# Performance work log

Measured on AMD Instinct MI355X. Metric: run time of the kernel, lower is better.

The kernel has to match this reference:

```python
import jax, jax.numpy as jnp
import numpy as np

B, T, D, H = 4, 2048, 1024, 16


def setup_inputs() -> dict:
    key = jax.random.key(0)
    ks = jax.random.split(key, 5)
    s = 0.02  # keep activations sane
    return {
        "x": jax.random.normal(ks[0], (B, T, D), jnp.float32),
        "Wq": jax.random.normal(ks[1], (D, D), jnp.float32) * s,
        "bq": jnp.zeros((D,), jnp.float32),
        "Wk": jax.random.normal(ks[2], (D, D), jnp.float32) * s,
        "bk": jnp.zeros((D,), jnp.float32),
        "Wv": jax.random.normal(ks[3], (D, D), jnp.float32) * s,
        "bv": jnp.zeros((D,), jnp.float32),
        "Wo": jax.random.normal(ks[4], (D, D), jnp.float32) * s,
        "bo": jnp.zeros((D,), jnp.float32),
    }


def _split_heads(t):  # (B,T,D) -> (B,H,T,d)
    b, s, d = t.shape
    return t.reshape(b, s, H, d // H).transpose(0, 2, 1, 3)


def reference(x, Wq, bq, Wk, bk, Wv, bv, Wo, bo):
    d_k = D // H
    q = _split_heads(x @ Wq + bq)  # (B,H,T,d)
    k = _split_heads(x @ Wk + bk)
    v = _split_heads(x @ Wv + bv)
    # scaled dot-product similarities (B,H,T,T)
    scores = jnp.einsum("bhqd,bhkd->bhqk", q, k) / jnp.sqrt(jnp.asarray(d_k, x.dtype))
    # causal mask: masked_fill(tril==0, -inf)
    causal = jnp.tril(jnp.ones((T, T), bool))
    scores = jnp.where(causal, scores, -jnp.inf)
    attn = jax.nn.softmax(scores, axis=-1)
    ctx = jnp.einsum("bhqk,bhkd->bhqd", attn, v)  # (B,H,T,d)
    ctx = ctx.transpose(0, 2, 1, 3).reshape(x.shape[0], T, D)
    return ctx @ Wo + bo
```

## Files before the change

kernel.cpp:

```cpp
#include <hip/hip_runtime.h>
#include <hip/hip_bf16.h>

typedef unsigned short u16;
typedef __attribute__((ext_vector_type(8))) short bf16x8;
typedef __attribute__((ext_vector_type(4))) short bf16x4;
typedef __attribute__((ext_vector_type(4))) float f32x4;

#define DD 1024
#define TT 2048
#define HH 16
#define BB 4
#define DK 64
#define MM 8192

#define QSCALE 0.180336880f

__device__ __forceinline__ u16 f2b(float x) {
  __hip_bfloat16 h = __float2bfloat16(x);
  return *reinterpret_cast<u16*>(&h);
}

__device__ __forceinline__ unsigned pk2(float a, float b) {
  float2 t; t.x = a; t.y = b;
  __hip_bfloat162 h = __float22bfloat162_rn(t);
  union { __hip_bfloat162 h; unsigned u; } cv;
  cv.h = h;
  return cv.u;
}

#define GLD16(gp, lp)                                                         \
  __builtin_amdgcn_global_load_lds(                                           \
      (const __attribute__((address_space(1))) unsigned int*)(gp),            \
      (__attribute__((address_space(3))) unsigned int*)(lp), 16, 0, 0)

__global__ __launch_bounds__(256) void cast_bf16_kernel(
    const float* __restrict__ src, u16* __restrict__ dst, int n) {
  int i = (blockIdx.x * 256 + threadIdx.x) * 4;
  if (i + 3 < n) {
    float4 v = *reinterpret_cast<const float4*>(src + i);
    ushort4 o;
    o.x = f2b(v.x); o.y = f2b(v.y); o.z = f2b(v.z); o.w = f2b(v.w);
    *reinterpret_cast<ushort4*>(dst + i) = o;
  }
}

__global__ __launch_bounds__(256) void transpose_cast_kernel(
    const float* __restrict__ W0, const float* __restrict__ W1,
    const float* __restrict__ W2, const float* __restrict__ W3,
    u16* __restrict__ O0, u16* __restrict__ O1,
    u16* __restrict__ O2, u16* __restrict__ O3) {
  const float* W; u16* O;
  switch (blockIdx.z) {
    case 0: W = W0; O = O0; break;
    case 1: W = W1; O = O1; break;
    case 2: W = W2; O = O2; break;
    default: W = W3; O = O3; break;
  }
  __shared__ float tile[32][33];
  int tx = threadIdx.x, ty = threadIdx.y;
  int bx = blockIdx.x * 32;
  int by = blockIdx.y * 32;
#pragma unroll
  for (int j = 0; j < 4; j++)
    tile[ty + j * 8][tx] = W[(size_t)(by + ty + j * 8) * DD + bx + tx];
  __syncthreads();
#pragma unroll
  for (int j = 0; j < 4; j++)
    O[(size_t)(bx + ty + j * 8) * DD + by + tx] = f2b(tile[tx][ty + j * 8]);
}

#define GEMM_STAGE(Aptr, Bptr, Asl, Bsl)                                      \
  _Pragma("unroll") for (int c = 0; c < 4; c++) {                             \
    int idx = tid * 8 + c * 2048;                                             \
    int row = idx >> 6, ck = idx & 63;                                        \
    int src = ck ^ ((row & 7) << 3);                                          \
    GLD16(Aptr + (size_t)(m0 + row) * DD + k0 + src, Asl + idx);              \
    GLD16(Bptr + (size_t)(n0 + row) * DD + k0 + src, Bsl + idx);              \
  }

#define GEMM_MFMA(Asl, Bsl)                                                   \
  _Pragma("unroll") for (int half = 0; half < 2; half++) {                    \
    bf16x8 af[4], bfr[4];                                                     \
    _Pragma("unroll") for (int mb = 0; mb < 4; mb++) {                        \
      int r = wm + mb * 16 + l16;                                             \
      af[mb] = *reinterpret_cast<const bf16x8*>(                              \
          &Asl[r * 64 + ((half * 32 + quad * 8) ^ ((r & 7) << 3))]);          \
    }                                                                         \
    _Pragma("unroll") for (int nb = 0; nb < 4; nb++) {                        \
      int r = wn + nb * 16 + l16;                                             \
      bfr[nb] = *reinterpret_cast<const bf16x8*>(                             \
          &Bsl[r * 64 + ((half * 32 + quad * 8) ^ ((r & 7) << 3))]);          \
    }                                                                         \
    _Pragma("unroll") for (int mb = 0; mb < 4; mb++)                          \
      _Pragma("unroll") for (int nb = 0; nb < 4; nb++)                        \
          acc[mb][nb] = __builtin_amdgcn_mfma_f32_16x16x32_bf16(              \
              af[mb], bfr[nb], acc[mb][nb], 0, 0, 0);                         \
  }

__global__ __launch_bounds__(256, 4) void gemm_qkv_kernel(
    const u16* __restrict__ A,
    const u16* __restrict__ WtQ, const u16* __restrict__ WtK,
    const u16* __restrict__ WtV,
    const float* __restrict__ bq, const float* __restrict__ bk,
    const float* __restrict__ bv,
    u16* __restrict__ Qo, u16* __restrict__ Ko, u16* __restrict__ Vo) {
  __shared__ __align__(16) u16 smem[17408];
  u16* As = smem;
  u16* Bs = smem + 8192;
  u16* Vs = smem;
  int z = blockIdx.z;
  const u16* Bt = (z == 0) ? WtQ : ((z == 1) ? WtK : WtV);
  const float* bias = (z == 0) ? bq : ((z == 1) ? bk : bv);
  int tid = threadIdx.x;
  int wave = tid >> 6, lane = tid & 63;
  int quad = lane >> 4, l16 = lane & 15;
  int m0 = blockIdx.x * 128, n0 = blockIdx.y * 128;
  int wm = (wave >> 1) * 64, wn = (wave & 1) * 64;

  f32x4 acc[4][4];
#pragma unroll
  for (int i = 0; i < 4; i++)
#pragma unroll
    for (int j = 0; j < 4; j++) acc[i][j] = (f32x4){0.f, 0.f, 0.f, 0.f};

  for (int k0 = 0; k0 < DD; k0 += 64) {
    GEMM_STAGE(A, Bt, As, Bs)
    __syncthreads();
    GEMM_MFMA(As, Bs)
    __syncthreads();
  }

  if (z == 2) {
#pragma unroll
    for (int mb = 0; mb < 4; mb++)
#pragma unroll
      for (int nb = 0; nb < 4; nb++) {
        int col = wn + nb * 16 + l16;
        float bv2 = bias[n0 + col];
#pragma unroll
        for (int r = 0; r < 4; r++) {
          int row = wm + mb * 16 + quad * 4 + r;
          Vs[col * 136 + row] = f2b(acc[mb][nb][r] + bv2);
        }
      }
    __syncthreads();
    int b = m0 >> 11;
    int tloc = m0 & 2047;
#pragma unroll
    for (int i = 0; i < 8; i++) {
      int idx = tid * 8 + i * 2048;
      int row = idx >> 7, col = idx & 127;
      uint4 v = *reinterpret_cast<const uint4*>(&Vs[row * 136 + col]);
      int ncol = n0 + row, h = ncol >> 6, dd = ncol & 63;
      *reinterpret_cast<uint4*>(
          Vo + (((size_t)(b * HH + h) * DK) + dd) * TT + tloc + col) = v;
    }
    return;
  }

  u16* outp = (z == 0) ? Qo : Ko;
  float scale = (z == 0) ? QSCALE : 1.0f;
#pragma unroll
  for (int mb = 0; mb < 4; mb++) {
#pragma unroll
    for (int nb = 0; nb < 4; nb++) {
      int col = n0 + wn + nb * 16 + l16;
      float bv2 = bias[col];
#pragma unroll
      for (int r = 0; r < 4; r++) {
        int row = m0 + wm + mb * 16 + quad * 4 + r;
        float val = (acc[mb][nb][r] + bv2) * scale;
        int hh = col >> 6, dd = col & 63;
        int b = row >> 11, t = row & 2047;
        outp[(((size_t)(b * HH + hh) * TT) + t) * DK + dd] = f2b(val);
      }
    }
  }
}

__global__ __launch_bounds__(256, 4) void gemm_out_kernel(
    const u16* __restrict__ A, const u16* __restrict__ Bt,
    const float* __restrict__ bias, float* __restrict__ outp) {
  __shared__ __align__(16) u16 As[128 * 64];
  __shared__ __align__(16) u16 Bs[128 * 64];
  int tid = threadIdx.x;
  int wave = tid >> 6, lane = tid & 63;
  int quad = lane >> 4, l16 = lane & 15;
  int m0 = blockIdx.x * 128, n0 = blockIdx.y * 128;
  int wm = (wave >> 1) * 64, wn = (wave & 1) * 64;

  f32x4 acc[4][4];
#pragma unroll
  for (int i = 0; i < 4; i++)
#pragma unroll
    for (int j = 0; j < 4; j++) acc[i][j] = (f32x4){0.f, 0.f, 0.f, 0.f};

  for (int k0 = 0; k0 < DD; k0 += 64) {
    GEMM_STAGE(A, Bt, As, Bs)
    __syncthreads();
    GEMM_MFMA(As, Bs)
    __syncthreads();
  }

#pragma unroll
  for (int mb = 0; mb < 4; mb++) {
#pragma unroll
    for (int nb = 0; nb < 4; nb++) {
      int col = n0 + wn + nb * 16 + l16;
      float bv = bias[col];
#pragma unroll
      for (int r = 0; r < 4; r++) {
        int row = m0 + wm + mb * 16 + quad * 4 + r;
        outp[(size_t)row * DD + col] = acc[mb][nb][r] + bv;
      }
    }
  }
}

__global__ __launch_bounds__(512, 4) void attn_kernel(
    const u16* __restrict__ Q, const u16* __restrict__ K,
    const u16* __restrict__ VT, u16* __restrict__ ctx) {
  __shared__ __align__(16) u16 Ks[2][128][72];
  __shared__ __align__(16) u16 Vt[2][64][136];

  int tid = threadIdx.x;
  int wave = tid >> 6, lane = tid & 63;
  int quad = lane >> 4, l16 = lane & 15;
  int bid = blockIdx.x;
  int bh = bid & 63;
  int px = bid >> 6;
  int b = bh >> 4, h = bh & 15;
  const u16* Qh = Q + (size_t)bh * TT * DK;
  const u16* Kh = K + (size_t)bh * TT * DK;
  const u16* Vh = VT + (size_t)bh * DK * TT;

  int ki0 = tid * 8, ki1 = tid * 8 + 4096;
  const bf16x4 ones = (bf16x4){0x3F80, 0x3F80, 0x3F80, 0x3F80};

  for (int phase = 0; phase < 2; phase++) {
    int qtc = phase ? px : (15 - px);
    __syncthreads();

    const u16* qrow = Qh + (size_t)(qtc * 128 + wave * 16 + l16) * DK + quad * 8;
    bf16x8 qf0 = *reinterpret_cast<const bf16x8*>(qrow);
    bf16x8 qf1 = *reinterpret_cast<const bf16x8*>(qrow + 32);

    uint4 kp0 = *reinterpret_cast<const uint4*>(Kh + ki0);
    uint4 kp1 = *reinterpret_cast<const uint4*>(Kh + ki1);
    uint4 vp0 = *reinterpret_cast<const uint4*>(Vh + (size_t)(ki0 >> 7) * TT + (ki0 & 127));
    uint4 vp1 = *reinterpret_cast<const uint4*>(Vh + (size_t)(ki1 >> 7) * TT + (ki1 & 127));
    *reinterpret_cast<uint4*>(&Ks[0][ki0 >> 6][ki0 & 63]) = kp0;
    *reinterpret_cast<uint4*>(&Ks[0][ki1 >> 6][ki1 & 63]) = kp1;
    *reinterpret_cast<uint4*>(&Vt[0][ki0 >> 7][ki0 & 127]) = vp0;
    *reinterpret_cast<uint4*>(&Vt[0][ki1 >> 7][ki1 & 127]) = vp1;
    __syncthreads();

    f32x4 oacc[4];
#pragma unroll
    for (int dt = 0; dt < 4; dt++) oacc[dt] = (f32x4){0.f, 0.f, 0.f, 0.f};
    f32x4 lacc = (f32x4){0.f, 0.f, 0.f, 0.f};

    for (int kt = 0; kt <= qtc; kt++) {
      int cur = kt & 1, nxt = cur ^ 1;
      bool more = kt < qtc;
      bool diag = kt == qtc;
      if (more) {
        kp0 = *reinterpret_cast<const uint4*>(Kh + (size_t)(kt + 1) * 8192 + ki0);
        kp1 = *reinterpret_cast<const uint4*>(Kh + (size_t)(kt + 1) * 8192 + ki1);
        vp0 = *reinterpret_cast<const uint4*>(
            Vh + (size_t)(ki0 >> 7) * TT + (kt + 1) * 128 + (ki0 & 127));
        vp1 = *reinterpret_cast<const uint4*>(
            Vh + (size_t)(ki1 >> 7) * TT + (kt + 1) * 128 + (ki1 & 127));
      }

#pragma unroll
      for (int kb = 0; kb < 8; kb++) {
        if (diag && kb > wave) continue;
        bf16x8 kf0 = *reinterpret_cast<const bf16x8*>(&Ks[cur][kb * 16 + l16][quad * 8]);
        bf16x8 kf1 = *reinterpret_cast<const bf16x8*>(&Ks[cur][kb * 16 + l16][32 + quad * 8]);
        f32x4 sacc = (f32x4){0.f, 0.f, 0.f, 0.f};
        sacc = __builtin_amdgcn_mfma_f32_16x16x32_bf16(kf0, qf0, sacc, 0, 0, 0);
        sacc = __builtin_amdgcn_mfma_f32_16x16x32_bf16(kf1, qf1, sacc, 0, 0, 0);
        if (diag && kb == wave) {
#pragma unroll
          for (int r = 0; r < 4; r++)
            if (quad * 4 + r > l16) sacc[r] = -__builtin_inff();
        }
        float p0 = __builtin_amdgcn_exp2f(sacc[0]);
        float p1 = __builtin_amdgcn_exp2f(sacc[1]);
        float p2 = __builtin_amdgcn_exp2f(sacc[2]);
        float p3 = __builtin_amdgcn_exp2f(sacc[3]);
        union { unsigned u[2]; bf16x4 v; } pk;
        pk.u[0] = pk2(p0, p1);
        pk.u[1] = pk2(p2, p3);
        lacc = __builtin_amdgcn_mfma_f32_16x16x16bf16_1k(pk.v, ones, lacc, 0, 0, 0);
#pragma unroll
        for (int dt = 0; dt < 4; dt++) {
          bf16x4 vf = *reinterpret_cast<const bf16x4*>(
              &Vt[cur][dt * 16 + l16][kb * 16 + quad * 4]);
          oacc[dt] = __builtin_amdgcn_mfma_f32_16x16x16bf16_1k(pk.v, vf, oacc[dt], 0, 0, 0);
        }
      }

      if (more) {
        *reinterpret_cast<uint4*>(&Ks[nxt][ki0 >> 6][ki0 & 63]) = kp0;
        *reinterpret_cast<uint4*>(&Ks[nxt][ki1 >> 6][ki1 & 63]) = kp1;
        *reinterpret_cast<uint4*>(&Vt[nxt][ki0 >> 7][ki0 & 127]) = vp0;
        *reinterpret_cast<uint4*>(&Vt[nxt][ki1 >> 7][ki1 & 127]) = vp1;
      }
      __syncthreads();
    }

    f32x4 inv;
#pragma unroll
    for (int r = 0; r < 4; r++) inv[r] = 1.0f / lacc[r];

    u16* Obuf = &Ks[0][0][0];
#pragma unroll
    for (int dt = 0; dt < 4; dt++)
#pragma unroll
      for (int r = 0; r < 4; r++)
        Obuf[(wave * 16 + quad * 4 + r) * 72 + dt * 16 + l16] =
            f2b(oacc[dt][r] * inv[r]);
    asm volatile("s_waitcnt lgkmcnt(0)" ::: "memory");
#pragma unroll
    for (int i = 0; i < 2; i++) {
      int idx = lane * 8 + i * 512;
      int row = idx >> 6, colc = idx & 63;
      uint4 v = *reinterpret_cast<const uint4*>(&Obuf[(wave * 16 + row) * 72 + colc]);
      int t = qtc * 128 + wave * 16 + row;
      *reinterpret_cast<uint4*>(
          ctx + ((size_t)(b * TT + t)) * DD + h * DK + colc) = v;
    }
  }
}

extern "C" void kernel_launch(void* const* d_in, const int* in_sizes, int n_in,
                              void* d_out, int out_size, void* d_ws, size_t ws_size,
                              hipStream_t stream) {
  const float* x  = (const float*)d_in[0];
  const float* Wq = (const float*)d_in[1];
  const float* bq = (const float*)d_in[2];
  const float* Wk = (const float*)d_in[3];
  const float* bk = (const float*)d_in[4];
  const float* Wv = (const float*)d_in[5];
  const float* bv = (const float*)d_in[6];
  const float* Wo = (const float*)d_in[7];
  const float* bo = (const float*)d_in[8];
  float* out = (float*)d_out;

  char* ws = (char*)d_ws;
  size_t off = 0;
  u16* xb  = (u16*)(ws + off); off += (size_t)MM * DD * 2;
  u16* wtq = (u16*)(ws + off); off += (size_t)DD * DD * 2;
  u16* wtk = (u16*)(ws + off); off += (size_t)DD * DD * 2;
  u16* wtv = (u16*)(ws + off); off += (size_t)DD * DD * 2;
  u16* wto = (u16*)(ws + off); off += (size_t)DD * DD * 2;
  u16* Qb  = (u16*)(ws + off); off += (size_t)MM * DD * 2;
  u16* Kb  = (u16*)(ws + off); off += (size_t)MM * DD * 2;
  u16* VTb = (u16*)(ws + off); off += (size_t)MM * DD * 2;
  u16* ctx = (u16*)(ws + off); off += (size_t)MM * DD * 2;

  {
    int n = MM * DD;
    cast_bf16_kernel<<<n / 1024, 256, 0, stream>>>(x, xb, n);
  }
  {
    dim3 grid(DD / 32, DD / 32, 4);
    dim3 block(32, 8);
    transpose_cast_kernel<<<grid, block, 0, stream>>>(Wq, Wk, Wv, Wo, wtq, wtk, wtv, wto);
  }
  {
    dim3 grid(MM / 128, DD / 128, 3);
    gemm_qkv_kernel<<<grid, 256, 0, stream>>>(xb, wtq, wtk, wtv, bq, bk, bv,
                                              Qb, Kb, VTb);
  }
  {
    attn_kernel<<<512, 512, 0, stream>>>(Qb, Kb, VTb, ctx);
  }
  {
    dim3 grid(MM / 128, DD / 128);
    gemm_out_kernel<<<grid, 256, 0, stream>>>(ctx, wto, bo, out);
  }
}
```

Before: 236.7 us.

## Give each attention wave two 16-row query sub-tiles to reuse K/V fragments

The attention kernel moves from 8 waves of 16 query rows to 4 waves of 32 rows each (256 threads per block). Each wave loads its K and V fragments from shared memory once per key block and reuses them for both query sub-tiles, which halves LDS reads per MFMA. The cost is more accumulator registers per wave and fewer waves per block to hide latency, and each thread now issues twice as many global loads for the K/V double-buffer fill.

```diff
diff --git a/kernel.cpp b/kernel.cpp
--- a/kernel.cpp
+++ b/kernel.cpp
@@ -217,7 +217,7 @@
   }
 }
 
-__global__ __launch_bounds__(512, 4) void attn_kernel(
+__global__ __launch_bounds__(256, 2) void attn_kernel(
     const u16* __restrict__ Q, const u16* __restrict__ K,
     const u16* __restrict__ VT, u16* __restrict__ ctx) {
   __shared__ __align__(16) u16 Ks[2][128][72];
@@ -234,101 +234,129 @@
   const u16* Kh = K + (size_t)bh * TT * DK;
   const u16* Vh = VT + (size_t)bh * DK * TT;
 
-  int ki0 = tid * 8, ki1 = tid * 8 + 4096;
   const bf16x4 ones = (bf16x4){0x3F80, 0x3F80, 0x3F80, 0x3F80};
 
   for (int phase = 0; phase < 2; phase++) {
     int qtc = phase ? px : (15 - px);
     __syncthreads();
 
-    const u16* qrow = Qh + (size_t)(qtc * 128 + wave * 16 + l16) * DK + quad * 8;
-    bf16x8 qf0 = *reinterpret_cast<const bf16x8*>(qrow);
-    bf16x8 qf1 = *reinterpret_cast<const bf16x8*>(qrow + 32);
-
-    uint4 kp0 = *reinterpret_cast<const uint4*>(Kh + ki0);
-    uint4 kp1 = *reinterpret_cast<const uint4*>(Kh + ki1);
-    uint4 vp0 = *reinterpret_cast<const uint4*>(Vh + (size_t)(ki0 >> 7) * TT + (ki0 & 127));
-    uint4 vp1 = *reinterpret_cast<const uint4*>(Vh + (size_t)(ki1 >> 7) * TT + (ki1 & 127));
-    *reinterpret_cast<uint4*>(&Ks[0][ki0 >> 6][ki0 & 63]) = kp0;
-    *reinterpret_cast<uint4*>(&Ks[0][ki1 >> 6][ki1 & 63]) = kp1;
-    *reinterpret_cast<uint4*>(&Vt[0][ki0 >> 7][ki0 & 127]) = vp0;
-    *reinterpret_cast<uint4*>(&Vt[0][ki1 >> 7][ki1 & 127]) = vp1;
-    __syncthreads();
-
-    f32x4 oacc[4];
-#pragma unroll
-    for (int dt = 0; dt < 4; dt++) oacc[dt] = (f32x4){0.f, 0.f, 0.f, 0.f};
-    f32x4 lacc = (f32x4){0.f, 0.f, 0.f, 0.f};
+    bf16x8 qf[2][2];
+#pragma unroll
+    for (int s = 0; s < 2; s++) {
+      const u16* qrow =
+          Qh + (size_t)(qtc * 128 + wave * 32 + s * 16 + l16) * DK + quad * 8;
+      qf[s][0] = *reinterpret_cast<const bf16x8*>(qrow);
+      qf[s][1] = *reinterpret_cast<const bf16x8*>(qrow + 32);
+    }
+
+    uint4 kp[4], vp[4];
+#pragma unroll
+    for (int c = 0; c < 4; c++) {
+      int idx = tid * 8 + c * 2048;
+      kp[c] = *reinterpret_cast<const uint4*>(Kh + idx);
+      vp[c] = *reinterpret_cast<const uint4*>(
+          Vh + (size_t)(idx >> 7) * TT + (idx & 127));
+      *reinterpret_cast<uint4*>(&Ks[0][idx >> 6][idx & 63]) = kp[c];
+      *reinterpret_cast<uint4*>(&Vt[0][idx >> 7][idx & 127]) = vp[c];
+    }
+    __syncthreads();
+
+    f32x4 oacc[2][4];
+    f32x4 lsum[2];
+#pragma unroll
+    for (int s = 0; s < 2; s++) {
+      lsum[s] = (f32x4){0.f, 0.f, 0.f, 0.f};
+#pragma unroll
+      for (int dt = 0; dt < 4; dt++) oacc[s][dt] = (f32x4){0.f, 0.f, 0.f, 0.f};
+    }
 
     for (int kt = 0; kt <= qtc; kt++) {
       int cur = kt & 1, nxt = cur ^ 1;
       bool more = kt < qtc;
       bool diag = kt == qtc;
       if (more) {
-        kp0 = *reinterpret_cast<const uint4*>(Kh + (size_t)(kt + 1) * 8192 + ki0);
-        kp1 = *reinterpret_cast<const uint4*>(Kh + (size_t)(kt + 1) * 8192 + ki1);
-        vp0 = *reinterpret_cast<const uint4*>(
-            Vh + (size_t)(ki0 >> 7) * TT + (kt + 1) * 128 + (ki0 & 127));
-        vp1 = *reinterpret_cast<const uint4*>(
-            Vh + (size_t)(ki1 >> 7) * TT + (kt + 1) * 128 + (ki1 & 127));
+#pragma unroll
+        for (int c = 0; c < 4; c++) {
+          int idx = tid * 8 + c * 2048;
+          kp[c] = *reinterpret_cast<const uint4*>(
+              Kh + (size_t)(kt + 1) * 8192 + idx);
+          vp[c] = *reinterpret_cast<const uint4*>(
+              Vh + (size_t)(idx >> 7) * TT + (kt + 1) * 128 + (idx & 127));
+        }
       }
 
 #pragma unroll
       for (int kb = 0; kb < 8; kb++) {
-        if (diag && kb > wave) continue;
-        bf16x8 kf0 = *reinterpret_cast<const bf16x8*>(&Ks[cur][kb * 16 + l16][quad * 8]);
-        bf16x8 kf1 = *reinterpret_cast<const bf16x8*>(&Ks[cur][kb * 16 + l16][32 + quad * 8]);
-        f32x4 sacc = (f32x4){0.f, 0.f, 0.f, 0.f};
-        sacc = __builtin_amdgcn_mfma_f32_16x16x32_bf16(kf0, qf0, sacc, 0, 0, 0);
-        sacc = __builtin_amdgcn_mfma_f32_16x16x32_bf16(kf1, qf1, sacc, 0, 0, 0);
-        if (diag && kb == wave) {
-#pragma unroll
-          for (int r = 0; r < 4; r++)
-            if (quad * 4 + r > l16) sacc[r] = -__builtin_inff();
+        if (diag && kb > 2 * wave + 1) continue;
+        bf16x8 kf0 =
+            *reinterpret_cast<const bf16x8*>(&Ks[cur][kb * 16 + l16][quad * 8]);
+        bf16x8 kf1 = *reinterpret_cast<const bf16x8*>(
+            &Ks[cur][kb * 16 + l16][32 + quad * 8]);
+        bf16x4 vf[4];
+#pragma unroll
+        for (int dt = 0; dt < 4; dt++)
+          vf[dt] = *reinterpret_cast<const bf16x4*>(
+              &Vt[cur][dt * 16 + l16][kb * 16 + quad * 4]);
+#pragma unroll
+        for (int s = 0; s < 2; s++) {
+          if (diag && kb > 2 * wave + s) continue;
+          f32x4 sacc = (f32x4){0.f, 0.f, 0.f, 0.f};
+          sacc = __builtin_amdgcn_mfma_f32_16x16x32_bf16(kf0, qf[s][0], sacc, 0, 0, 0);
+          sacc = __builtin_amdgcn_mfma_f32_16x16x32_bf16(kf1, qf[s][1], sacc, 0, 0, 0);
+          if (diag && kb == 2 * wave + s) {
+#pragma unroll
+            for (int r = 0; r < 4; r++)
+              if (quad * 4 + r > l16) sacc[r] = -__builtin_inff();
+          }
+          float p0 = __builtin_amdgcn_exp2f(sacc[0]);
+          float p1 = __builtin_amdgcn_exp2f(sacc[1]);
+          float p2 = __builtin_amdgcn_exp2f(sacc[2]);
+          float p3 = __builtin_amdgcn_exp2f(sacc[3]);
+          union { unsigned u[2]; bf16x4 v; } pk;
+          pk.u[0] = pk2(p0, p1);
+          pk.u[1] = pk2(p2, p3);
+          lsum[s] = __builtin_amdgcn_mfma_f32_16x16x16bf16_1k(pk.v, ones, lsum[s], 0, 0, 0);
+#pragma unroll
+          for (int dt = 0; dt < 4; dt++)
+            oacc[s][dt] = __builtin_amdgcn_mfma_f32_16x16x16bf16_1k(
+                pk.v, vf[dt], oacc[s][dt], 0, 0, 0);
         }
-        float p0 = __builtin_amdgcn_exp2f(sacc[0]);
-        float p1 = __builtin_amdgcn_exp2f(sacc[1]);
-        float p2 = __builtin_amdgcn_exp2f(sacc[2]);
-        float p3 = __builtin_amdgcn_exp2f(sacc[3]);
-        union { unsigned u[2]; bf16x4 v; } pk;
-        pk.u[0] = pk2(p0, p1);
-        pk.u[1] = pk2(p2, p3);
-        lacc = __builtin_amdgcn_mfma_f32_16x16x16bf16_1k(pk.v, ones, lacc, 0, 0, 0);
-#pragma unroll
-        for (int dt = 0; dt < 4; dt++) {
-          bf16x4 vf = *reinterpret_cast<const bf16x4*>(
-              &Vt[cur][dt * 16 + l16][kb * 16 + quad * 4]);
-          oacc[dt] = __builtin_amdgcn_mfma_f32_16x16x16bf16_1k(pk.v, vf, oacc[dt], 0, 0, 0);
+      }
+
+      if (more) {
+#pragma unroll
+        for (int c = 0; c < 4; c++) {
+          int idx = tid * 8 + c * 2048;
+          *reinterpret_cast<uint4*>(&Ks[nxt][idx >> 6][idx & 63]) = kp[c];
+          *reinterpret_cast<uint4*>(&Vt[nxt][idx >> 7][idx & 127]) = vp[c];
         }
       }
-
-      if (more) {
-        *reinterpret_cast<uint4*>(&Ks[nxt][ki0 >> 6][ki0 & 63]) = kp0;
-        *reinterpret_cast<uint4*>(&Ks[nxt][ki1 >> 6][ki1 & 63]) = kp1;
-        *reinterpret_cast<uint4*>(&Vt[nxt][ki0 >> 7][ki0 & 127]) = vp0;
-        *reinterpret_cast<uint4*>(&Vt[nxt][ki1 >> 7][ki1 & 127]) = vp1;
-      }
       __syncthreads();
     }
 
-    f32x4 inv;
-#pragma unroll
-    for (int r = 0; r < 4; r++) inv[r] = 1.0f / lacc[r];
+    f32x4 inv[2];
+#pragma unroll
+    for (int s = 0; s < 2; s++)
+#pragma unroll
+      for (int r = 0; r < 4; r++) inv[s][r] = 1.0f / lsum[s][r];
 
     u16* Obuf = &Ks[0][0][0];
 #pragma unroll
-    for (int dt = 0; dt < 4; dt++)
-#pragma unroll
-      for (int r = 0; r < 4; r++)
-        Obuf[(wave * 16 + quad * 4 + r) * 72 + dt * 16 + l16] =
-            f2b(oacc[dt][r] * inv[r]);
+    for (int s = 0; s < 2; s++)
+#pragma unroll
+      for (int dt = 0; dt < 4; dt++)
+#pragma unroll
+        for (int r = 0; r < 4; r++)
+          Obuf[(wave * 32 + s * 16 + quad * 4 + r) * 72 + dt * 16 + l16] =
+              f2b(oacc[s][dt][r] * inv[s][r]);
     asm volatile("s_waitcnt lgkmcnt(0)" ::: "memory");
 #pragma unroll
-    for (int i = 0; i < 2; i++) {
+    for (int i = 0; i < 4; i++) {
       int idx = lane * 8 + i * 512;
       int row = idx >> 6, colc = idx & 63;
-      uint4 v = *reinterpret_cast<const uint4*>(&Obuf[(wave * 16 + row) * 72 + colc]);
-      int t = qtc * 128 + wave * 16 + row;
+      uint4 v =
+          *reinterpret_cast<const uint4*>(&Obuf[(wave * 32 + row) * 72 + colc]);
+      int t = qtc * 128 + wave * 32 + row;
       *reinterpret_cast<uint4*>(
           ctx + ((size_t)(b * TT + t)) * DD + h * DK + colc) = v;
     }
@@ -376,7 +404,7 @@
                                               Qb, Kb, VTb);
   }
   {
-    attn_kernel<<<512, 512, 0, stream>>>(Qb, Kb, VTb, ctx);
+    attn_kernel<<<512, 256, 0, stream>>>(Qb, Kb, VTb, ctx);
   }
   {
     dim3 grid(MM / 128, DD / 128);
```

Result: slower. 280.8 us (+18.6%).
